# Optimization experiments

Hardware: AMD Instinct MI355X
Metric: run time of the kernel (lower is better)

## Reference

```python
import jax, jax.numpy as jnp
import numpy as np


def setup_inputs() -> dict:
    key = jax.random.key(0)
    x = jax.random.normal(key, (128, 256, 32, 32), dtype=jnp.float32)
    return {"x": x, "iter_num": 5}


def reference(x, iter_num):
    # x: (B, C, H, W)
    B, C, H, W = x.shape
    N = H * W
    xr = x.reshape(B, C, N)
    # Covariance pooling: X @ I_hat @ X^T == (1/N) * Xc @ Xc^T  (I_hat = I/N - J/N^2)
    xc = xr - xr.mean(axis=2, keepdims=True)
    cov = jnp.einsum('bcn,bdn->bcd', xc, xc) / N  # (B, C, C)

    # Newton-Schulz iterative matrix square root
    I = jnp.eye(C, dtype=x.dtype)
    I3 = 3.0 * I
    trace = jnp.trace(cov, axis1=1, axis2=2)[:, None, None]  # norm_A = tr(cov)
    A = cov / trace
    ZY = 0.5 * (I3 - A)
    Y = A @ ZY
    Z = ZY
    for _ in range(1, iter_num - 1):
        ZY = 0.5 * (I3 - Z @ Y)
        Y = Y @ ZY
        Z = ZY @ Z
    YZY = 0.5 * (Y @ (I3 - Z @ Y))
    sqrtm = YZY * jnp.sqrt(trace)  # (B, C, C)

    # Upper-triangular vectorization (row-major, including diagonal)
    r, c = np.triu_indices(C)
    idx = jnp.asarray(r * C + c)
    return sqrtm.reshape(B, C * C)[:, idx]  # (B, C*(C+1)//2)
```

## Files before the change

### kernel.cpp

```cpp
#include <hip/hip_runtime.h>
#include <hip/hip_fp16.h>


typedef _Float16 half8 __attribute__((ext_vector_type(8)));
typedef _Float16 half4 __attribute__((ext_vector_type(4)));
typedef float f32x4 __attribute__((ext_vector_type(4)));

#define OUTPB 32896

__device__ __forceinline__ void gl_lds16(const void* g, void* l) {
  __builtin_amdgcn_global_load_lds(
      (const __attribute__((address_space(1))) void*)g,
      (__attribute__((address_space(3))) void*)l, 16, 0, 0);
}

#define VMB(N) asm volatile("s_waitcnt vmcnt(" #N ")\n\ts_barrier" ::: "memory")
#define LKB()  asm volatile("s_waitcnt lgkmcnt(0)\n\ts_barrier" ::: "memory")

__device__ __forceinline__ void tile_pq(int t, int& p, int& q) {
  p = (t > 3) + (t > 6) + (t > 8);
  int base = p * 4 - (p * (p - 1)) / 2;
  q = p + (t - base);
}

__device__ __forceinline__ void mfma64(const _Float16* lA, const _Float16* lB,
                                       f32x4 (&acc)[2][2], int wr, int wc,
                                       int lr, int lk) {
#pragma unroll
  for (int ks = 0; ks < 2; ++ks) {
    half8 af[2], bf[2];
#pragma unroll
    for (int m = 0; m < 2; ++m) {
      int row = wr * 32 + m * 16 + lr;
      int kc = (ks * 4 + lk) ^ (row & 7);
      af[m] = *(const half8*)&lA[row * 64 + kc * 8];
    }
#pragma unroll
    for (int n = 0; n < 2; ++n) {
      int row = wc * 32 + n * 16 + lr;
      int kc = (ks * 4 + lk) ^ (row & 7);
      bf[n] = *(const half8*)&lB[row * 64 + kc * 8];
    }
    __builtin_amdgcn_s_setprio(1);
#pragma unroll
    for (int m = 0; m < 2; ++m)
#pragma unroll
      for (int n = 0; n < 2; ++n)
        acc[m][n] = __builtin_amdgcn_mfma_f32_16x16x32_f16(af[m], bf[n], acc[m][n], 0, 0, 0);
    __builtin_amdgcn_s_setprio(0);
  }
}

template <typename F>
__device__ __forceinline__ void store_sym(F f, _Float16* D, size_t boff, int p, int q,
    bool mirror, _Float16* ldsT, f32x4 (&acc)[2][2],
    int wr, int wc, int lr, int lk, int tid) {
#pragma unroll
  for (int m = 0; m < 2; ++m)
#pragma unroll
    for (int n = 0; n < 2; ++n) {
      int il0 = wr * 32 + m * 16 + lk * 4;
      int jl = wc * 32 + n * 16 + lr;
      half4 v4;
#pragma unroll
      for (int r = 0; r < 4; ++r) {
        _Float16 v = f(acc[m][n][r], p * 64 + il0 + r, q * 64 + jl);
        v4[r] = v;
        if (mirror) ldsT[(il0 + r) * 64 + (jl ^ (((il0 + r) & 7) << 3))] = v;
      }
      *(half4*)&D[boff + (size_t)(q * 64 + jl) * 256 + p * 64 + il0] = v4;
    }
  if (mirror) {
    __syncthreads();
#pragma unroll
    for (int pp = 0; pp < 2; ++pp) {
      int u = pp * 256 + tid;
      int im = u >> 3, cu = u & 7;
      half8 v8 = *(const half8*)&ldsT[im * 64 + ((cu ^ (im & 7)) << 3)];
      *(half8*)&D[boff + (size_t)(p * 64 + im) * 256 + q * 64 + cu * 8] = v8;
    }
  }
}

__global__ __launch_bounds__(256) void k_center(const float* __restrict__ x,
                                                _Float16* __restrict__ xc) {
  int gw = blockIdx.x * 4 + (threadIdx.x >> 6);
  int lane = threadIdx.x & 63;
#pragma unroll 1
  for (int rr = 0; rr < 4; ++rr) {
    int r = gw * 4 + rr;
    const float4* rp = (const float4*)(x + (size_t)r * 1024);
    float4 v0 = rp[2 * lane], v1 = rp[2 * lane + 1];
    float4 v2 = rp[128 + 2 * lane], v3 = rp[128 + 2 * lane + 1];
    float s = v0.x + v0.y + v0.z + v0.w + v1.x + v1.y + v1.z + v1.w +
              v2.x + v2.y + v2.z + v2.w + v3.x + v3.y + v3.z + v3.w;
#pragma unroll
    for (int o = 1; o < 64; o <<= 1) s += __shfl_xor(s, o);
    float mn = s * (1.f / 1024.f);
    _Float16* orow = xc + (size_t)r * 1024;
    half8 h;
    h[0] = (_Float16)(v0.x - mn); h[1] = (_Float16)(v0.y - mn);
    h[2] = (_Float16)(v0.z - mn); h[3] = (_Float16)(v0.w - mn);
    h[4] = (_Float16)(v1.x - mn); h[5] = (_Float16)(v1.y - mn);
    h[6] = (_Float16)(v1.z - mn); h[7] = (_Float16)(v1.w - mn);
    *(half8*)&orow[lane * 8] = h;
    h[0] = (_Float16)(v2.x - mn); h[1] = (_Float16)(v2.y - mn);
    h[2] = (_Float16)(v2.z - mn); h[3] = (_Float16)(v2.w - mn);
    h[4] = (_Float16)(v3.x - mn); h[5] = (_Float16)(v3.y - mn);
    h[6] = (_Float16)(v3.z - mn); h[7] = (_Float16)(v3.w - mn);
    *(half8*)&orow[512 + lane * 8] = h;
  }
}

__global__ __launch_bounds__(256, 4) void k_covg(const _Float16* __restrict__ xc,
                                                 _Float16* __restrict__ covh,
                                                 float* __restrict__ trPart) {
  __shared__ _Float16 lds[16384];
  __shared__ float sred[4];

  const int lin = blockIdx.x + 10 * blockIdx.y;
  const int cid = (lin & 7) * 160 + (lin >> 3);
  const int b = cid / 10, t = cid - 10 * b;
  int p, q; tile_pq(t, p, q);
  const bool diag = (p == q);
  const int tid = threadIdx.x, w = tid >> 6, lane = tid & 63;
  const int wr = w >> 1, wc = w & 1, lr = lane & 15, lk = lane >> 4;

  const _Float16* Ap = xc + ((size_t)b * 256 + p * 64) * 1024;
  const _Float16* Bp = xc + ((size_t)b * 256 + q * 64) * 1024;

  f32x4 acc[2][2] = {};

  auto stageH = [&](const _Float16* panel, int buf, int base, int kk) {
#pragma unroll
    for (int i = 0; i < 2; ++i) {
      int s = (w * 2 + i) * 64 + lane;
      int row = s >> 3, cst = s & 7;
      int kc = cst ^ (row & 7);
      gl_lds16(panel + (size_t)row * 1024 + kk * 64 + kc * 8,
               &lds[base + buf * 4096 + (w * 2 + i) * 512]);
    }
  };

  stageH(Ap, 0, 0, 0);
  if (!diag) stageH(Bp, 0, 8192, 0);
#pragma unroll 1
  for (int kk = 0; kk < 16; ++kk) {
    int cur = kk & 1;
    if (kk < 15) {
      stageH(Ap, cur ^ 1, 0, kk + 1);
      if (!diag) {
        stageH(Bp, cur ^ 1, 8192, kk + 1);
        VMB(4);
      } else {
        VMB(2);
      }
    } else {
      VMB(0);
    }
    mfma64(&lds[cur * 4096], diag ? &lds[cur * 4096] : &lds[8192 + cur * 4096],
           acc, wr, wc, lr, lk);
    LKB();
  }

  const float inv = 1.f / 1024.f;
  if (diag) {
    float tp = 0.f;
#pragma unroll
    for (int m = 0; m < 2; ++m)
#pragma unroll
      for (int n = 0; n < 2; ++n)
#pragma unroll
        for (int r = 0; r < 4; ++r) {
          int il = wr * 32 + m * 16 + lk * 4 + r, jl = wc * 32 + n * 16 + lr;
          if (il == jl) tp += acc[m][n][r] * inv;
        }
#pragma unroll
    for (int o = 32; o; o >>= 1) tp += __shfl_down(tp, o);
    if (lane == 0) sred[w] = tp;
    __syncthreads();
    if (tid == 0) trPart[b * 4 + p] = sred[0] + sred[1] + sred[2] + sred[3];
    __syncthreads();
  }

  store_sym([&](float a, int i, int j) { return (_Float16)(a * inv); },
            covh, (size_t)b * 65536, p, q, !diag, lds, acc, wr, wc, lr, lk, tid);
}

enum { EPI_S2 = 0, EPI_ZY = 1, EPI_OUT = 2 };

struct GP {
  const _Float16 *A0, *B0;
  _Float16 *D0, *D1;
  const _Float16* covh;
  const float* trP;
  float* outF;
};

template <int EPI>
__global__ __launch_bounds__(256, 4) void k_gemm(GP g) {
  __shared__ _Float16 lds[16384];

  const int lin = blockIdx.x + 10 * blockIdx.y;
  const int cid = (lin & 7) * 160 + (lin >> 3);
  const int b = cid / 10, t = cid - 10 * b;
  int p, q; tile_pq(t, p, q);
  const bool diag = (p == q);
  const bool share = diag && (EPI == EPI_S2);
  const int tid = threadIdx.x, w = tid >> 6, lane = tid & 63;
  const int wr = w >> 1, wc = w & 1, lr = lane & 15, lk = lane >> 4;

  const size_t boff = (size_t)b * 65536;
  const _Float16* Ap = g.A0 + boff + (size_t)p * 64 * 256;
  const _Float16* Bp = ((EPI == EPI_S2) ? g.A0 : g.B0) + boff + (size_t)q * 64 * 256;

  f32x4 acc[2][2] = {};

  auto stageH = [&](const _Float16* panel, int buf, int base, int kk) {
#pragma unroll
    for (int i = 0; i < 2; ++i) {
      int s = (w * 2 + i) * 64 + lane;
      int row = s >> 3, cst = s & 7;
      int kc = cst ^ (row & 7);
      gl_lds16(panel + (size_t)row * 256 + kk * 64 + kc * 8,
               &lds[base + buf * 4096 + (w * 2 + i) * 512]);
    }
  };

  stageH(Ap, 0, 0, 0);
  if (!share) stageH(Bp, 0, 8192, 0);
#pragma unroll 1
  for (int kk = 0; kk < 4; ++kk) {
    int cur = kk & 1;
    if (kk < 3) {
      stageH(Ap, cur ^ 1, 0, kk + 1);
      if (!share) {
        stageH(Bp, cur ^ 1, 8192, kk + 1);
        VMB(4);
      } else {
        VMB(2);
      }
    } else {
      VMB(0);
    }
    mfma64(&lds[cur * 4096], share ? &lds[cur * 4096] : &lds[8192 + cur * 4096],
           acc, wr, wc, lr, lk);
    LKB();
  }

  if constexpr (EPI == EPI_ZY) {
    store_sym([&](float a, int i, int j) {
                return (_Float16)((i == j ? 1.5f : 0.f) - 0.5f * a);
              }, g.D0, boff, p, q, !diag, lds, acc, wr, wc, lr, lk, tid);
  } else if constexpr (EPI == EPI_S2) {
    float tv = g.trP[b * 4] + g.trP[b * 4 + 1] + g.trP[b * 4 + 2] + g.trP[b * 4 + 3];
    float it1 = 1.f / tv;
    _Float16* TY = lds;
    _Float16* TZ = lds + 4096;
#pragma unroll
    for (int m = 0; m < 2; ++m)
#pragma unroll
      for (int n = 0; n < 2; ++n) {
        int il0 = wr * 32 + m * 16 + lk * 4;
        int jl = wc * 32 + n * 16 + lr;
        half4 c4 = *(const half4*)&g.covh[boff + (size_t)(q * 64 + jl) * 256 + p * 64 + il0];
        half4 y4, z4;
#pragma unroll
        for (int r = 0; r < 4; ++r) {
          int i = p * 64 + il0 + r, j = q * 64 + jl;
          float c = (float)c4[r];
          y4[r] = (_Float16)(1.5f * c * it1 - 0.5f * acc[m][n][r] * it1 * it1);
          z4[r] = (_Float16)((i == j ? 1.5f : 0.f) - 0.5f * c * it1);
          if (!diag) {
            int sp = (il0 + r) * 64 + (jl ^ (((il0 + r) & 7) << 3));
            TY[sp] = y4[r]; TZ[sp] = z4[r];
          }
        }
        *(half4*)&g.D0[boff + (size_t)(q * 64 + jl) * 256 + p * 64 + il0] = y4;
        *(half4*)&g.D1[boff + (size_t)(q * 64 + jl) * 256 + p * 64 + il0] = z4;
      }
    if (!diag) {
      __syncthreads();
#pragma unroll
      for (int pp = 0; pp < 2; ++pp) {
        int u = pp * 256 + tid;
        int im = u >> 3, cu = u & 7;
        half8 vy = *(const half8*)&TY[im * 64 + ((cu ^ (im & 7)) << 3)];
        half8 vz = *(const half8*)&TZ[im * 64 + ((cu ^ (im & 7)) << 3)];
        *(half8*)&g.D0[boff + (size_t)(p * 64 + im) * 256 + q * 64 + cu * 8] = vy;
        *(half8*)&g.D1[boff + (size_t)(p * 64 + im) * 256 + q * 64 + cu * 8] = vz;
      }
    }
  } else {
    float tv = g.trP[b * 4] + g.trP[b * 4 + 1] + g.trP[b * 4 + 2] + g.trP[b * 4 + 3];
    float st = sqrtf(tv);
#pragma unroll
    for (int m = 0; m < 2; ++m)
#pragma unroll
      for (int n = 0; n < 2; ++n)
#pragma unroll
        for (int r = 0; r < 4; ++r) {
          int i = p * 64 + wr * 32 + m * 16 + lk * 4 + r;
          int j = q * 64 + wc * 32 + n * 16 + lr;
          if (i <= j) {
            int idx = j + i * 256 - (i * (i + 1)) / 2;
            g.outF[(size_t)b * OUTPB + idx] = acc[m][n][r] * st;
          }
        }
  }
}

struct YZP {
  const _Float16 *Y, *Z, *W;
  _Float16 *Yn, *Zn;
};

__global__ __launch_bounds__(256, 4) void k_yzm(YZP g) {
  __shared__ _Float16 lds[24576];

  const int lin = blockIdx.x + 10 * blockIdx.y;
  const int cid = (lin & 7) * 160 + (lin >> 3);
  const int b = cid / 10, t = cid - 10 * b;
  int p, q; tile_pq(t, p, q);
  const bool diag = (p == q);
  const int tid = threadIdx.x, w = tid >> 6, lane = tid & 63;
  const int wr = w >> 1, wc = w & 1, lr = lane & 15, lk = lane >> 4;

  const size_t boff = (size_t)b * 65536;
  const _Float16* Yp = g.Y + boff + (size_t)p * 64 * 256;
  const _Float16* Zp = g.Z + boff + (size_t)p * 64 * 256;
  const _Float16* Wp = g.W + boff + (size_t)q * 64 * 256;

  f32x4 accY[2][2] = {}, accZ[2][2] = {};

  auto stageH = [&](const _Float16* panel, int buf, int base, int kk) {
#pragma unroll
    for (int i = 0; i < 2; ++i) {
      int s = (w * 2 + i) * 64 + lane;
      int row = s >> 3, cst = s & 7;
      int kc = cst ^ (row & 7);
      gl_lds16(panel + (size_t)row * 256 + kk * 64 + kc * 8,
               &lds[base + buf * 4096 + (w * 2 + i) * 512]);
    }
  };

  auto step = [&](const _Float16* lY, const _Float16* lZ, const _Float16* lW) {
#pragma unroll
    for (int ks = 0; ks < 2; ++ks) {
      half8 yf[2], zf[2], wf[2];
#pragma unroll
      for (int m = 0; m < 2; ++m) {
        int row = wr * 32 + m * 16 + lr;
        int kc = (ks * 4 + lk) ^ (row & 7);
        yf[m] = *(const half8*)&lY[row * 64 + kc * 8];
        zf[m] = *(const half8*)&lZ[row * 64 + kc * 8];
      }
#pragma unroll
      for (int n = 0; n < 2; ++n) {
        int row = wc * 32 + n * 16 + lr;
        int kc = (ks * 4 + lk) ^ (row & 7);
        wf[n] = *(const half8*)&lW[row * 64 + kc * 8];
      }
      __builtin_amdgcn_s_setprio(1);
#pragma unroll
      for (int m = 0; m < 2; ++m)
#pragma unroll
        for (int n = 0; n < 2; ++n) {
          accY[m][n] = __builtin_amdgcn_mfma_f32_16x16x32_f16(yf[m], wf[n], accY[m][n], 0, 0, 0);
          accZ[m][n] = __builtin_amdgcn_mfma_f32_16x16x32_f16(zf[m], wf[n], accZ[m][n], 0, 0, 0);
        }
      __builtin_amdgcn_s_setprio(0);
    }
  };

  stageH(Yp, 0, 0, 0); stageH(Zp, 0, 8192, 0); stageH(Wp, 0, 16384, 0);
#pragma unroll 1
  for (int kk = 0; kk < 4; ++kk) {
    int cur = kk & 1;
    if (kk < 3) {
      stageH(Yp, cur ^ 1, 0, kk + 1);
      stageH(Zp, cur ^ 1, 8192, kk + 1);
      stageH(Wp, cur ^ 1, 16384, kk + 1);
      VMB(6);
    } else {
      VMB(0);
    }
    step(&lds[cur * 4096], &lds[8192 + cur * 4096], &lds[16384 + cur * 4096]);
    LKB();
  }

  _Float16* TY = lds;
  _Float16* TZ = lds + 4096;
#pragma unroll
  for (int m = 0; m < 2; ++m)
#pragma unroll
    for (int n = 0; n < 2; ++n) {
      int il0 = wr * 32 + m * 16 + lk * 4;
      int jl = wc * 32 + n * 16 + lr;
      half4 y4, z4;
#pragma unroll
      for (int r = 0; r < 4; ++r) {
        y4[r] = (_Float16)accY[m][n][r];
        z4[r] = (_Float16)accZ[m][n][r];
        if (!diag) {
          int sp = (il0 + r) * 64 + (jl ^ (((il0 + r) & 7) << 3));
          TY[sp] = y4[r]; TZ[sp] = z4[r];
        }
      }
      *(half4*)&g.Yn[boff + (size_t)(q * 64 + jl) * 256 + p * 64 + il0] = y4;
      *(half4*)&g.Zn[boff + (size_t)(q * 64 + jl) * 256 + p * 64 + il0] = z4;
    }
  if (!diag) {
    __syncthreads();
#pragma unroll
    for (int pp = 0; pp < 2; ++pp) {
      int u = pp * 256 + tid;
      int im = u >> 3, cu = u & 7;
      half8 vy = *(const half8*)&TY[im * 64 + ((cu ^ (im & 7)) << 3)];
      half8 vz = *(const half8*)&TZ[im * 64 + ((cu ^ (im & 7)) << 3)];
      *(half8*)&g.Yn[boff + (size_t)(p * 64 + im) * 256 + q * 64 + cu * 8] = vy;
      *(half8*)&g.Zn[boff + (size_t)(p * 64 + im) * 256 + q * 64 + cu * 8] = vz;
    }
  }
}

extern "C" void kernel_launch(void* const* d_in, const int* in_sizes, int n_in,
                              void* d_out, int out_size, void* d_ws, size_t ws_size,
                              hipStream_t stream) {
  const float* x = (const float*)d_in[0];
  float* outF = (float*)d_out;

  char* ws = (char*)d_ws;
  const size_t MATB = (size_t)128 * 65536 * sizeof(_Float16);
  _Float16* xc   = (_Float16*)ws;
  _Float16* Y0   = (_Float16*)ws;
  _Float16* Z0   = (_Float16*)(ws + MATB);
  _Float16* Y1   = (_Float16*)(ws + 2 * MATB);
  _Float16* Z1   = (_Float16*)(ws + 3 * MATB);
  _Float16* covh = (_Float16*)(ws + 4 * MATB);
  float* trP     = (float*)(ws + 5 * MATB);

  dim3 g10(10, 128);

  k_center<<<2048, 256, 0, stream>>>(x, xc);
  k_covg<<<g10, 256, 0, stream>>>(xc, covh, trP);

  {
    GP a{};
    a.A0 = covh; a.D0 = Y0; a.D1 = Z0;
    a.covh = covh; a.trP = trP;
    k_gemm<EPI_S2><<<g10, 256, 0, stream>>>(a);
  }

  _Float16 *Yc = Y0, *Zc = Z0, *Yn = Y1, *Zn = Z1;
  for (int itn = 0; itn < 3; ++itn) {
    GP a{};
    a.A0 = Zc; a.B0 = Yc; a.D0 = covh;
    k_gemm<EPI_ZY><<<g10, 256, 0, stream>>>(a);
    YZP r{};
    r.Y = Yc; r.Z = Zc; r.W = covh; r.Yn = Yn; r.Zn = Zn;
    k_yzm<<<g10, 256, 0, stream>>>(r);
    _Float16* t0 = Yc; Yc = Yn; Yn = t0;
    _Float16* t1 = Zc; Zc = Zn; Zn = t1;
  }
  {
    GP a{};
    a.A0 = Zc; a.B0 = Yc; a.D0 = covh;
    k_gemm<EPI_ZY><<<g10, 256, 0, stream>>>(a);
    GP o{};
    o.A0 = Yc; o.B0 = covh; o.trP = trP; o.outF = outF;
    k_gemm<EPI_OUT><<<g10, 256, 0, stream>>>(o);
  }
}
```

Baseline: 179.4 us.

## Fuse all pipeline stages into one persistent cooperative kernel with grid syncs

Replaces the sequence of eleven kernel launches with a single persistent cooperative kernel of 768 blocks that runs centering, covariance, Newton-Schulz iterations and output stages in turn, separated by grid-wide syncs. Each block processes one or two tile tasks per stage. The aim is to remove launch overhead and inter-kernel gaps. In exchange, occupancy is capped at 3 blocks per CU, the second task round is uneven across blocks, and each grid sync costs something. The old multi-kernel path remains as a fallback.

```diff
diff --git a/kernel.cpp b/kernel.cpp
--- a/kernel.cpp
+++ b/kernel.cpp
@@ -1,5 +1,8 @@
 #include <hip/hip_runtime.h>
 #include <hip/hip_fp16.h>
+#include <hip/hip_cooperative_groups.h>
+
+namespace cg = cooperative_groups;
 
 
 typedef _Float16 half8 __attribute__((ext_vector_type(8)));
@@ -82,13 +85,49 @@
   }
 }
 
-__global__ __launch_bounds__(256) void k_center(const float* __restrict__ x,
-                                                _Float16* __restrict__ xc) {
-  int gw = blockIdx.x * 4 + (threadIdx.x >> 6);
+__device__ __forceinline__ void gemm64(const _Float16* Ap, const _Float16* Bp,
+    int strideH, int ksteps, bool share, _Float16* lds, f32x4 (&acc)[2][2], int tid) {
+  const int w = tid >> 6, lane = tid & 63;
+  const int wr = w >> 1, wc = w & 1, lr = lane & 15, lk = lane >> 4;
+
+  auto stageH = [&](const _Float16* panel, int buf, int base, int kk) {
+#pragma unroll
+    for (int i = 0; i < 2; ++i) {
+      int s = (w * 2 + i) * 64 + lane;
+      int row = s >> 3, cst = s & 7;
+      int kc = cst ^ (row & 7);
+      gl_lds16(panel + (size_t)row * strideH + kk * 64 + kc * 8,
+               &lds[base + buf * 4096 + (w * 2 + i) * 512]);
+    }
+  };
+
+  stageH(Ap, 0, 0, 0);
+  if (!share) stageH(Bp, 0, 8192, 0);
+#pragma unroll 1
+  for (int kk = 0; kk < ksteps; ++kk) {
+    int cur = kk & 1;
+    if (kk + 1 < ksteps) {
+      stageH(Ap, cur ^ 1, 0, kk + 1);
+      if (!share) {
+        stageH(Bp, cur ^ 1, 8192, kk + 1);
+        VMB(4);
+      } else {
+        VMB(2);
+      }
+    } else {
+      VMB(0);
+    }
+    mfma64(&lds[cur * 4096], share ? &lds[cur * 4096] : &lds[8192 + cur * 4096],
+           acc, wr, wc, lr, lk);
+    LKB();
+  }
+}
+
+__device__ __forceinline__ void center_rows(const float* x, _Float16* xc,
+                                            int gw, int nw) {
   int lane = threadIdx.x & 63;
 #pragma unroll 1
-  for (int rr = 0; rr < 4; ++rr) {
-    int r = gw * 4 + rr;
+  for (int r = gw; r < 32768; r += nw) {
     const float4* rp = (const float4*)(x + (size_t)r * 1024);
     float4 v0 = rp[2 * lane], v1 = rp[2 * lane + 1];
     float4 v2 = rp[128 + 2 * lane], v3 = rp[128 + 2 * lane + 1];
@@ -112,59 +151,22 @@
   }
 }
 
-__global__ __launch_bounds__(256, 4) void k_covg(const _Float16* __restrict__ xc,
-                                                 _Float16* __restrict__ covh,
-                                                 float* __restrict__ trPart) {
-  __shared__ _Float16 lds[16384];
-  __shared__ float sred[4];
-
-  const int lin = blockIdx.x + 10 * blockIdx.y;
-  const int cid = (lin & 7) * 160 + (lin >> 3);
-  const int b = cid / 10, t = cid - 10 * b;
+__device__ __forceinline__ void stage_cov(int task, const _Float16* xc,
+    _Float16* covh, float* trPart, _Float16* lds, int tid) {
+  const int b = task / 10, t = task - 10 * b;
   int p, q; tile_pq(t, p, q);
   const bool diag = (p == q);
-  const int tid = threadIdx.x, w = tid >> 6, lane = tid & 63;
+  const int w = tid >> 6, lane = tid & 63;
   const int wr = w >> 1, wc = w & 1, lr = lane & 15, lk = lane >> 4;
 
   const _Float16* Ap = xc + ((size_t)b * 256 + p * 64) * 1024;
   const _Float16* Bp = xc + ((size_t)b * 256 + q * 64) * 1024;
-
   f32x4 acc[2][2] = {};
-
-  auto stageH = [&](const _Float16* panel, int buf, int base, int kk) {
-#pragma unroll
-    for (int i = 0; i < 2; ++i) {
-      int s = (w * 2 + i) * 64 + lane;
-      int row = s >> 3, cst = s & 7;
-      int kc = cst ^ (row & 7);
-      gl_lds16(panel + (size_t)row * 1024 + kk * 64 + kc * 8,
-               &lds[base + buf * 4096 + (w * 2 + i) * 512]);
-    }
-  };
-
-  stageH(Ap, 0, 0, 0);
-  if (!diag) stageH(Bp, 0, 8192, 0);
-#pragma unroll 1
-  for (int kk = 0; kk < 16; ++kk) {
-    int cur = kk & 1;
-    if (kk < 15) {
-      stageH(Ap, cur ^ 1, 0, kk + 1);
-      if (!diag) {
-        stageH(Bp, cur ^ 1, 8192, kk + 1);
-        VMB(4);
-      } else {
-        VMB(2);
-      }
-    } else {
-      VMB(0);
-    }
-    mfma64(&lds[cur * 4096], diag ? &lds[cur * 4096] : &lds[8192 + cur * 4096],
-           acc, wr, wc, lr, lk);
-    LKB();
-  }
+  gemm64(Ap, Bp, 1024, 16, diag, lds, acc, tid);
 
   const float inv = 1.f / 1024.f;
   if (diag) {
+    float* sred = (float*)(lds + 16384);
     float tp = 0.f;
 #pragma unroll
     for (int m = 0; m < 2; ++m)
@@ -180,41 +182,95 @@
     if (lane == 0) sred[w] = tp;
     __syncthreads();
     if (tid == 0) trPart[b * 4 + p] = sred[0] + sred[1] + sred[2] + sred[3];
-    __syncthreads();
-  }
-
+  }
   store_sym([&](float a, int i, int j) { return (_Float16)(a * inv); },
             covh, (size_t)b * 65536, p, q, !diag, lds, acc, wr, wc, lr, lk, tid);
 }
 
-enum { EPI_S2 = 0, EPI_ZY = 1, EPI_OUT = 2 };
-
-struct GP {
-  const _Float16 *A0, *B0;
-  _Float16 *D0, *D1;
-  const _Float16* covh;
-  const float* trP;
-  float* outF;
-};
-
-template <int EPI>
-__global__ __launch_bounds__(256, 4) void k_gemm(GP g) {
-  __shared__ _Float16 lds[16384];
-
-  const int lin = blockIdx.x + 10 * blockIdx.y;
-  const int cid = (lin & 7) * 160 + (lin >> 3);
-  const int b = cid / 10, t = cid - 10 * b;
+__device__ __forceinline__ void stage_s2(int task, const _Float16* covh,
+    const float* trP, _Float16* Y0, _Float16* Z0, _Float16* lds, int tid) {
+  const int b = task / 10, t = task - 10 * b;
   int p, q; tile_pq(t, p, q);
   const bool diag = (p == q);
-  const bool share = diag && (EPI == EPI_S2);
-  const int tid = threadIdx.x, w = tid >> 6, lane = tid & 63;
+  const int w = tid >> 6, lane = tid & 63;
   const int wr = w >> 1, wc = w & 1, lr = lane & 15, lk = lane >> 4;
-
   const size_t boff = (size_t)b * 65536;
-  const _Float16* Ap = g.A0 + boff + (size_t)p * 64 * 256;
-  const _Float16* Bp = ((EPI == EPI_S2) ? g.A0 : g.B0) + boff + (size_t)q * 64 * 256;
 
   f32x4 acc[2][2] = {};
+  gemm64(covh + boff + (size_t)p * 64 * 256, covh + boff + (size_t)q * 64 * 256,
+         256, 4, diag, lds, acc, tid);
+
+  float tv = trP[b * 4] + trP[b * 4 + 1] + trP[b * 4 + 2] + trP[b * 4 + 3];
+  float it1 = 1.f / tv;
+  _Float16* TY = lds;
+  _Float16* TZ = lds + 4096;
+#pragma unroll
+  for (int m = 0; m < 2; ++m)
+#pragma unroll
+    for (int n = 0; n < 2; ++n) {
+      int il0 = wr * 32 + m * 16 + lk * 4;
+      int jl = wc * 32 + n * 16 + lr;
+      half4 c4 = *(const half4*)&covh[boff + (size_t)(q * 64 + jl) * 256 + p * 64 + il0];
+      half4 y4, z4;
+#pragma unroll
+      for (int r = 0; r < 4; ++r) {
+        int i = p * 64 + il0 + r, j = q * 64 + jl;
+        float c = (float)c4[r];
+        y4[r] = (_Float16)(1.5f * c * it1 - 0.5f * acc[m][n][r] * it1 * it1);
+        z4[r] = (_Float16)((i == j ? 1.5f : 0.f) - 0.5f * c * it1);
+        if (!diag) {
+          int sp = (il0 + r) * 64 + (jl ^ (((il0 + r) & 7) << 3));
+          TY[sp] = y4[r]; TZ[sp] = z4[r];
+        }
+      }
+      *(half4*)&Y0[boff + (size_t)(q * 64 + jl) * 256 + p * 64 + il0] = y4;
+      *(half4*)&Z0[boff + (size_t)(q * 64 + jl) * 256 + p * 64 + il0] = z4;
+    }
+  if (!diag) {
+    __syncthreads();
+#pragma unroll
+    for (int pp = 0; pp < 2; ++pp) {
+      int u = pp * 256 + tid;
+      int im = u >> 3, cu = u & 7;
+      half8 vy = *(const half8*)&TY[im * 64 + ((cu ^ (im & 7)) << 3)];
+      half8 vz = *(const half8*)&TZ[im * 64 + ((cu ^ (im & 7)) << 3)];
+      *(half8*)&Y0[boff + (size_t)(p * 64 + im) * 256 + q * 64 + cu * 8] = vy;
+      *(half8*)&Z0[boff + (size_t)(p * 64 + im) * 256 + q * 64 + cu * 8] = vz;
+    }
+  }
+}
+
+__device__ __forceinline__ void stage_zy(int task, const _Float16* Z,
+    const _Float16* Y, _Float16* W, _Float16* lds, int tid) {
+  const int b = task / 10, t = task - 10 * b;
+  int p, q; tile_pq(t, p, q);
+  const bool diag = (p == q);
+  const int w = tid >> 6, lane = tid & 63;
+  const int wr = w >> 1, wc = w & 1, lr = lane & 15, lk = lane >> 4;
+  const size_t boff = (size_t)b * 65536;
+
+  f32x4 acc[2][2] = {};
+  gemm64(Z + boff + (size_t)p * 64 * 256, Y + boff + (size_t)q * 64 * 256,
+         256, 4, false, lds, acc, tid);
+  store_sym([&](float a, int i, int j) {
+              return (_Float16)((i == j ? 1.5f : 0.f) - 0.5f * a);
+            }, W, boff, p, q, !diag, lds, acc, wr, wc, lr, lk, tid);
+}
+
+__device__ __forceinline__ void stage_yzm(int task, const _Float16* Y,
+    const _Float16* Z, const _Float16* W, _Float16* Yn, _Float16* Zn,
+    _Float16* lds, int tid) {
+  const int b = task / 10, t = task - 10 * b;
+  int p, q; tile_pq(t, p, q);
+  const bool diag = (p == q);
+  const int w = tid >> 6, lane = tid & 63;
+  const int wr = w >> 1, wc = w & 1, lr = lane & 15, lk = lane >> 4;
+  const size_t boff = (size_t)b * 65536;
+
+  const _Float16* Yp = Y + boff + (size_t)p * 64 * 256;
+  const _Float16* Zp = Z + boff + (size_t)p * 64 * 256;
+  const _Float16* Wp = W + boff + (size_t)q * 64 * 256;
+  f32x4 accY[2][2] = {}, accZ[2][2] = {};
 
   auto stageH = [&](const _Float16* panel, int buf, int base, int kk) {
 #pragma unroll
@@ -226,124 +282,6 @@
                &lds[base + buf * 4096 + (w * 2 + i) * 512]);
     }
   };
-
-  stageH(Ap, 0, 0, 0);
-  if (!share) stageH(Bp, 0, 8192, 0);
-#pragma unroll 1
-  for (int kk = 0; kk < 4; ++kk) {
-    int cur = kk & 1;
-    if (kk < 3) {
-      stageH(Ap, cur ^ 1, 0, kk + 1);
-      if (!share) {
-        stageH(Bp, cur ^ 1, 8192, kk + 1);
-        VMB(4);
-      } else {
-        VMB(2);
-      }
-    } else {
-      VMB(0);
-    }
-    mfma64(&lds[cur * 4096], share ? &lds[cur * 4096] : &lds[8192 + cur * 4096],
-           acc, wr, wc, lr, lk);
-    LKB();
-  }
-
-  if constexpr (EPI == EPI_ZY) {
-    store_sym([&](float a, int i, int j) {
-                return (_Float16)((i == j ? 1.5f : 0.f) - 0.5f * a);
-              }, g.D0, boff, p, q, !diag, lds, acc, wr, wc, lr, lk, tid);
-  } else if constexpr (EPI == EPI_S2) {
-    float tv = g.trP[b * 4] + g.trP[b * 4 + 1] + g.trP[b * 4 + 2] + g.trP[b * 4 + 3];
-    float it1 = 1.f / tv;
-    _Float16* TY = lds;
-    _Float16* TZ = lds + 4096;
-#pragma unroll
-    for (int m = 0; m < 2; ++m)
-#pragma unroll
-      for (int n = 0; n < 2; ++n) {
-        int il0 = wr * 32 + m * 16 + lk * 4;
-        int jl = wc * 32 + n * 16 + lr;
-        half4 c4 = *(const half4*)&g.covh[boff + (size_t)(q * 64 + jl) * 256 + p * 64 + il0];
-        half4 y4, z4;
-#pragma unroll
-        for (int r = 0; r < 4; ++r) {
-          int i = p * 64 + il0 + r, j = q * 64 + jl;
-          float c = (float)c4[r];
-          y4[r] = (_Float16)(1.5f * c * it1 - 0.5f * acc[m][n][r] * it1 * it1);
-          z4[r] = (_Float16)((i == j ? 1.5f : 0.f) - 0.5f * c * it1);
-          if (!diag) {
-            int sp = (il0 + r) * 64 + (jl ^ (((il0 + r) & 7) << 3));
-            TY[sp] = y4[r]; TZ[sp] = z4[r];
-          }
-        }
-        *(half4*)&g.D0[boff + (size_t)(q * 64 + jl) * 256 + p * 64 + il0] = y4;
-        *(half4*)&g.D1[boff + (size_t)(q * 64 + jl) * 256 + p * 64 + il0] = z4;
-      }
-    if (!diag) {
-      __syncthreads();
-#pragma unroll
-      for (int pp = 0; pp < 2; ++pp) {
-        int u = pp * 256 + tid;
-        int im = u >> 3, cu = u & 7;
-        half8 vy = *(const half8*)&TY[im * 64 + ((cu ^ (im & 7)) << 3)];
-        half8 vz = *(const half8*)&TZ[im * 64 + ((cu ^ (im & 7)) << 3)];
-        *(half8*)&g.D0[boff + (size_t)(p * 64 + im) * 256 + q * 64 + cu * 8] = vy;
-        *(half8*)&g.D1[boff + (size_t)(p * 64 + im) * 256 + q * 64 + cu * 8] = vz;
-      }
-    }
-  } else {
-    float tv = g.trP[b * 4] + g.trP[b * 4 + 1] + g.trP[b * 4 + 2] + g.trP[b * 4 + 3];
-    float st = sqrtf(tv);
-#pragma unroll
-    for (int m = 0; m < 2; ++m)
-#pragma unroll
-      for (int n = 0; n < 2; ++n)
-#pragma unroll
-        for (int r = 0; r < 4; ++r) {
-          int i = p * 64 + wr * 32 + m * 16 + lk * 4 + r;
-          int j = q * 64 + wc * 32 + n * 16 + lr;
-          if (i <= j) {
-            int idx = j + i * 256 - (i * (i + 1)) / 2;
-            g.outF[(size_t)b * OUTPB + idx] = acc[m][n][r] * st;
-          }
-        }
-  }
-}
-
-struct YZP {
-  const _Float16 *Y, *Z, *W;
-  _Float16 *Yn, *Zn;
-};
-
-__global__ __launch_bounds__(256, 4) void k_yzm(YZP g) {
-  __shared__ _Float16 lds[24576];
-
-  const int lin = blockIdx.x + 10 * blockIdx.y;
-  const int cid = (lin & 7) * 160 + (lin >> 3);
-  const int b = cid / 10, t = cid - 10 * b;
-  int p, q; tile_pq(t, p, q);
-  const bool diag = (p == q);
-  const int tid = threadIdx.x, w = tid >> 6, lane = tid & 63;
-  const int wr = w >> 1, wc = w & 1, lr = lane & 15, lk = lane >> 4;
-
-  const size_t boff = (size_t)b * 65536;
-  const _Float16* Yp = g.Y + boff + (size_t)p * 64 * 256;
-  const _Float16* Zp = g.Z + boff + (size_t)p * 64 * 256;
-  const _Float16* Wp = g.W + boff + (size_t)q * 64 * 256;
-
-  f32x4 accY[2][2] = {}, accZ[2][2] = {};
-
-  auto stageH = [&](const _Float16* panel, int buf, int base, int kk) {
-#pragma unroll
-    for (int i = 0; i < 2; ++i) {
-      int s = (w * 2 + i) * 64 + lane;
-      int row = s >> 3, cst = s & 7;
-      int kc = cst ^ (row & 7);
-      gl_lds16(panel + (size_t)row * 256 + kk * 64 + kc * 8,
-               &lds[base + buf * 4096 + (w * 2 + i) * 512]);
-    }
-  };
-
   auto step = [&](const _Float16* lY, const _Float16* lZ, const _Float16* lW) {
 #pragma unroll
     for (int ks = 0; ks < 2; ++ks) {
@@ -407,8 +345,8 @@
           TY[sp] = y4[r]; TZ[sp] = z4[r];
         }
       }
-      *(half4*)&g.Yn[boff + (size_t)(q * 64 + jl) * 256 + p * 64 + il0] = y4;
-      *(half4*)&g.Zn[boff + (size_t)(q * 64 + jl) * 256 + p * 64 + il0] = z4;
+      *(half4*)&Yn[boff + (size_t)(q * 64 + jl) * 256 + p * 64 + il0] = y4;
+      *(half4*)&Zn[boff + (size_t)(q * 64 + jl) * 256 + p * 64 + il0] = z4;
     }
   if (!diag) {
     __syncthreads();
@@ -418,10 +356,126 @@
       int im = u >> 3, cu = u & 7;
       half8 vy = *(const half8*)&TY[im * 64 + ((cu ^ (im & 7)) << 3)];
       half8 vz = *(const half8*)&TZ[im * 64 + ((cu ^ (im & 7)) << 3)];
-      *(half8*)&g.Yn[boff + (size_t)(p * 64 + im) * 256 + q * 64 + cu * 8] = vy;
-      *(half8*)&g.Zn[boff + (size_t)(p * 64 + im) * 256 + q * 64 + cu * 8] = vz;
-    }
-  }
+      *(half8*)&Yn[boff + (size_t)(p * 64 + im) * 256 + q * 64 + cu * 8] = vy;
+      *(half8*)&Zn[boff + (size_t)(p * 64 + im) * 256 + q * 64 + cu * 8] = vz;
+    }
+  }
+}
+
+__device__ __forceinline__ void stage_out(int task, const _Float16* Y,
+    const _Float16* W, const float* trP, float* outF, _Float16* lds, int tid) {
+  const int b = task / 10, t = task - 10 * b;
+  int p, q; tile_pq(t, p, q);
+  const int w = tid >> 6, lane = tid & 63;
+  const int wr = w >> 1, wc = w & 1, lr = lane & 15, lk = lane >> 4;
+  const size_t boff = (size_t)b * 65536;
+
+  f32x4 acc[2][2] = {};
+  gemm64(Y + boff + (size_t)p * 64 * 256, W + boff + (size_t)q * 64 * 256,
+         256, 4, false, lds, acc, tid);
+  float tv = trP[b * 4] + trP[b * 4 + 1] + trP[b * 4 + 2] + trP[b * 4 + 3];
+  float st = sqrtf(tv);
+#pragma unroll
+  for (int m = 0; m < 2; ++m)
+#pragma unroll
+    for (int n = 0; n < 2; ++n)
+#pragma unroll
+      for (int r = 0; r < 4; ++r) {
+        int i = p * 64 + wr * 32 + m * 16 + lk * 4 + r;
+        int j = q * 64 + wc * 32 + n * 16 + lr;
+        if (i <= j) {
+          int idx = j + i * 256 - (i * (i + 1)) / 2;
+          outF[(size_t)b * OUTPB + idx] = acc[m][n][r] * st;
+        }
+      }
+}
+
+struct MP {
+  const float* x;
+  _Float16 *xc, *Y0, *Z0, *Y1, *Z1, *covh;
+  float* trP;
+  float* outF;
+};
+
+#define RUN_TASKS(STAGE_CALL)                                \
+  {                                                          \
+    int task = x8 * 160 + j8;                                \
+    STAGE_CALL;                                              \
+    if (j8 < 64) {                                           \
+      __syncthreads();                                       \
+      task += 96;                                            \
+      STAGE_CALL;                                            \
+    }                                                        \
+  }
+
+__global__ __launch_bounds__(256, 3) void k_mega(MP P) {
+  __shared__ _Float16 lds[24576];
+  cg::grid_group grid = cg::this_grid();
+  const int tid = threadIdx.x;
+  const int bid = blockIdx.x;
+  const int x8 = bid & 7, j8 = bid >> 3;
+
+  center_rows(P.x, P.xc, bid * 4 + (tid >> 6), 3072);
+  __threadfence(); grid.sync();
+
+  RUN_TASKS(stage_cov(task, P.xc, P.covh, P.trP, lds, tid));
+  __threadfence(); grid.sync();
+
+  RUN_TASKS(stage_s2(task, P.covh, P.trP, P.Y0, P.Z0, lds, tid));
+  __threadfence(); grid.sync();
+
+  const _Float16 *Yc = P.Y0, *Zc = P.Z0;
+  _Float16 *Yn = P.Y1, *Zn = P.Z1;
+#pragma unroll 1
+  for (int itn = 0; itn < 3; ++itn) {
+    RUN_TASKS(stage_zy(task, Zc, Yc, P.covh, lds, tid));
+    __threadfence(); grid.sync();
+    RUN_TASKS(stage_yzm(task, Yc, Zc, P.covh, Yn, Zn, lds, tid));
+    __threadfence(); grid.sync();
+    const _Float16* ty = Yc; Yc = Yn; Yn = (_Float16*)ty;
+    const _Float16* tz = Zc; Zc = Zn; Zn = (_Float16*)tz;
+  }
+
+  RUN_TASKS(stage_zy(task, Zc, Yc, P.covh, lds, tid));
+  __threadfence(); grid.sync();
+
+  RUN_TASKS(stage_out(task, Yc, P.covh, P.trP, P.outF, lds, tid));
+}
+
+__device__ __forceinline__ int swz_cid() {
+  int lin = blockIdx.x + 10 * blockIdx.y;
+  return (lin & 7) * 160 + (lin >> 3);
+}
+
+__global__ __launch_bounds__(256) void k_centerF(const float* __restrict__ x,
+                                                 _Float16* __restrict__ xc) {
+  center_rows(x, xc, blockIdx.x * 4 + (threadIdx.x >> 6), 8192);
+}
+__global__ __launch_bounds__(256, 3) void k_covF(const _Float16* xc, _Float16* covh,
+                                                 float* trP) {
+  __shared__ _Float16 lds[24576];
+  stage_cov(swz_cid(), xc, covh, trP, lds, threadIdx.x);
+}
+__global__ __launch_bounds__(256, 3) void k_s2F(const _Float16* covh, const float* trP,
+                                                _Float16* Y0, _Float16* Z0) {
+  __shared__ _Float16 lds[24576];
+  stage_s2(swz_cid(), covh, trP, Y0, Z0, lds, threadIdx.x);
+}
+__global__ __launch_bounds__(256, 3) void k_zyF(const _Float16* Z, const _Float16* Y,
+                                                _Float16* W) {
+  __shared__ _Float16 lds[24576];
+  stage_zy(swz_cid(), Z, Y, W, lds, threadIdx.x);
+}
+__global__ __launch_bounds__(256, 3) void k_yzmF(const _Float16* Y, const _Float16* Z,
+                                                 const _Float16* W, _Float16* Yn,
+                                                 _Float16* Zn) {
+  __shared__ _Float16 lds[24576];
+  stage_yzm(swz_cid(), Y, Z, W, Yn, Zn, lds, threadIdx.x);
+}
+__global__ __launch_bounds__(256, 3) void k_outF(const _Float16* Y, const _Float16* W,
+                                                 const float* trP, float* outF) {
+  __shared__ _Float16 lds[24576];
+  stage_out(swz_cid(), Y, W, trP, outF, lds, threadIdx.x);
 }
 
 extern "C" void kernel_launch(void* const* d_in, const int* in_sizes, int n_in,
@@ -432,43 +486,38 @@
 
   char* ws = (char*)d_ws;
   const size_t MATB = (size_t)128 * 65536 * sizeof(_Float16);
-  _Float16* xc   = (_Float16*)ws;
-  _Float16* Y0   = (_Float16*)ws;
-  _Float16* Z0   = (_Float16*)(ws + MATB);
-  _Float16* Y1   = (_Float16*)(ws + 2 * MATB);
-  _Float16* Z1   = (_Float16*)(ws + 3 * MATB);
-  _Float16* covh = (_Float16*)(ws + 4 * MATB);
-  float* trP     = (float*)(ws + 5 * MATB);
+  MP P;
+  P.x = x;
+  P.xc   = (_Float16*)ws;
+  P.Y0   = (_Float16*)ws;
+  P.Z0   = (_Float16*)(ws + MATB);
+  P.Y1   = (_Float16*)(ws + 2 * MATB);
+  P.Z1   = (_Float16*)(ws + 3 * MATB);
+  P.covh = (_Float16*)(ws + 4 * MATB);
+  P.trP  = (float*)(ws + 5 * MATB);
+  P.outF = outF;
+
+  int maxb = 0;
+  hipError_t qe = hipOccupancyMaxActiveBlocksPerMultiprocessor(&maxb, k_mega, 256, 0);
+  if (qe == hipSuccess && maxb >= 3 && ws_size >= 5 * MATB + 4096) {
+    void* args[] = {&P};
+    if (hipLaunchCooperativeKernel((const void*)k_mega, dim3(768), dim3(256),
+                                   args, 0, stream) == hipSuccess)
+      return;
+    (void)hipGetLastError();
+  }
 
   dim3 g10(10, 128);
-
-  k_center<<<2048, 256, 0, stream>>>(x, xc);
-  k_covg<<<g10, 256, 0, stream>>>(xc, covh, trP);
-
-  {
-    GP a{};
-    a.A0 = covh; a.D0 = Y0; a.D1 = Z0;
-    a.covh = covh; a.trP = trP;
-    k_gemm<EPI_S2><<<g10, 256, 0, stream>>>(a);
-  }
-
-  _Float16 *Yc = Y0, *Zc = Z0, *Yn = Y1, *Zn = Z1;
+  k_centerF<<<2048, 256, 0, stream>>>(x, P.xc);
+  k_covF<<<g10, 256, 0, stream>>>(P.xc, P.covh, P.trP);
+  k_s2F<<<g10, 256, 0, stream>>>(P.covh, P.trP, P.Y0, P.Z0);
+  _Float16 *Yc = P.Y0, *Zc = P.Z0, *Yn = P.Y1, *Zn = P.Z1;
   for (int itn = 0; itn < 3; ++itn) {
-    GP a{};
-    a.A0 = Zc; a.B0 = Yc; a.D0 = covh;
-    k_gemm<EPI_ZY><<<g10, 256, 0, stream>>>(a);
-    YZP r{};
-    r.Y = Yc; r.Z = Zc; r.W = covh; r.Yn = Yn; r.Zn = Zn;
-    k_yzm<<<g10, 256, 0, stream>>>(r);
+    k_zyF<<<g10, 256, 0, stream>>>(Zc, Yc, P.covh);
+    k_yzmF<<<g10, 256, 0, stream>>>(Yc, Zc, P.covh, Yn, Zn);
     _Float16* t0 = Yc; Yc = Yn; Yn = t0;
     _Float16* t1 = Zc; Zc = Zn; Zn = t1;
   }
-  {
-    GP a{};
-    a.A0 = Zc; a.B0 = Yc; a.D0 = covh;
-    k_gemm<EPI_ZY><<<g10, 256, 0, stream>>>(a);
-    GP o{};
-    o.A0 = Yc; o.B0 = covh; o.trP = trP; o.outF = outF;
-    k_gemm<EPI_OUT><<<g10, 256, 0, stream>>>(o);
-  }
-}
+  k_zyF<<<g10, 256, 0, stream>>>(Zc, Yc, P.covh);
+  k_outF<<<g10, 256, 0, stream>>>(Yc, P.covh, P.trP, outF);
+}
```

Result: no change. 176.9 us (-1.4%).
